# Kernel tuning notes

Hardware: AMD Instinct MI355X
Metric: run time of the kernel (lower is better)

Reference implementation:

```python
import jax, jax.numpy as jnp
import numpy as np

N = 50000        # num nodes
E = 1600000      # num edges (before self loops)
F_IN = 128
F_OUT = 64
SLOPE = 0.2      # PyG GATConv default negative_slope


def setup_inputs() -> dict:
    key = jax.random.key(0)
    k0, k1, k2, k3, k4, k5 = jax.random.split(key, 6)
    x = jax.random.normal(k0, (N, F_IN), dtype=jnp.float32)
    # GATConv params (heads=1): linear weight, attention vectors, bias
    W = jax.random.normal(k1, (F_IN, F_OUT), dtype=jnp.float32) * (1.0 / np.sqrt(F_IN))
    a_src = jax.random.normal(k2, (F_OUT,), dtype=jnp.float32) * (1.0 / np.sqrt(F_OUT))
    a_dst = jax.random.normal(k3, (F_OUT,), dtype=jnp.float32) * (1.0 / np.sqrt(F_OUT))
    bias = jax.random.normal(k4, (F_OUT,), dtype=jnp.float32) * 0.01
    edge_index = jax.random.randint(k5, (2, E), 0, N, dtype=jnp.int32)
    return {"x": x, "W": W, "a_src": a_src, "a_dst": a_dst, "bias": bias,
            "edge_index": edge_index}


def reference(x, W, a_src, a_dst, bias, edge_index):
    # Linear transform: [N, F_OUT]
    xp = x @ W
    # add self loops (PyG GATConv default add_self_loops=True)
    loop = jnp.arange(N, dtype=edge_index.dtype)
    src = jnp.concatenate([edge_index[0], loop])  # source j of edge j->i
    dst = jnp.concatenate([edge_index[1], loop])  # target i
    # per-node attention logits, gathered per edge
    alpha_s = xp @ a_src  # [N]
    alpha_d = xp @ a_dst  # [N]
    e = alpha_s[src] + alpha_d[dst]               # [E+N]
    e = jnp.where(e > 0, e, SLOPE * e)            # leaky_relu(0.2)
    # segment softmax over edges grouped by destination node
    emax = jax.ops.segment_max(e, dst, num_segments=N)  # every node has a self loop
    w = jnp.exp(e - emax[dst])
    denom = jax.ops.segment_sum(w, dst, num_segments=N)
    alpha = w / denom[dst]                        # [E+N]
    # scatter-aggregate weighted source features
    out = jax.ops.segment_sum(alpha[:, None] * xp[src], dst, num_segments=N)
    out = out + bias
    # F.relu then unsqueeze(dim=0) and cat with empty -> [1, N, F_OUT]
    return jax.nn.relu(out)[None, :, :]
```

## Files before the change

### kernel.cpp

```cpp
#include <hip/hip_runtime.h>
#include <hip/hip_fp16.h>
#include <math.h>

#define N_NODES 50000
#define N_EDGES 1600000
#define ET (N_EDGES + N_NODES)
#define F_OUT 64
#define F_IN 128
#define SLOPE 0.2f
#define BSHIFT 7
#define BNODES 128
#define NBUCK ((N_NODES + BNODES - 1) >> BSHIFT)
#define CAP 4736
#define EPB 4096
#define PBLOCKS ((ET + EPB - 1) / EPB)

typedef _Float16 half8 __attribute__((ext_vector_type(8)));
typedef _Float16 half4 __attribute__((ext_vector_type(4)));
typedef float f32x4 __attribute__((ext_vector_type(4)));

__global__ __launch_bounds__(256) void gemm_kernel(const float4* __restrict__ x4,
                                                   const float* __restrict__ W,
                                                   const float* __restrict__ a_src,
                                                   const float* __restrict__ a_dst,
                                                   _Float16* __restrict__ xph,
                                                   float* __restrict__ alpha_s,
                                                   float* __restrict__ alpha_d,
                                                   int* __restrict__ bcur) {
    __shared__ _Float16 xs[64][136];
    int t = threadIdx.x;
    if (blockIdx.x == 0)
        for (int i = t; i < NBUCK; i += 256) bcur[i] = 0;
    int wave = t >> 6, lane = t & 63;
    int g = lane >> 4, c16 = lane & 15;

    size_t rbase = (size_t)blockIdx.x * 64;
#pragma unroll
    for (int i = 0; i < 8; ++i) {
        int idx = t + i * 256;
        int row = idx >> 5, c4 = idx & 31;
        size_t gr = rbase + row;
        if (gr >= N_NODES) gr = N_NODES - 1;
        float4 v = x4[gr * (F_IN / 4) + c4];
        half4 hv = { (_Float16)v.x, (_Float16)v.y, (_Float16)v.z, (_Float16)v.w };
        *(half4*)&xs[row][c4 * 4] = hv;
    }

    half8 bw[4][4];
#pragma unroll
    for (int nt = 0; nt < 4; ++nt)
#pragma unroll
        for (int kt = 0; kt < 4; ++kt) {
            int col = nt * 16 + c16;
            int k0 = kt * 32 + g * 8;
#pragma unroll
            for (int e = 0; e < 8; ++e)
                bw[nt][kt][e] = (_Float16)W[(k0 + e) * F_OUT + col];
        }
    __syncthreads();

    int r0 = wave * 16;
    half8 af[4];
#pragma unroll
    for (int kt = 0; kt < 4; ++kt)
        af[kt] = *(const half8*)&xs[r0 + c16][kt * 32 + g * 8];

    f32x4 acc[4];
#pragma unroll
    for (int nt = 0; nt < 4; ++nt) {
        acc[nt] = (f32x4){0.f, 0.f, 0.f, 0.f};
#pragma unroll
        for (int kt = 0; kt < 4; ++kt)
            acc[nt] = __builtin_amdgcn_mfma_f32_16x16x32_f16(af[kt], bw[nt][kt], acc[nt], 0, 0, 0);
    }

    int growbase = (int)rbase + r0 + g * 4;
#pragma unroll
    for (int nt = 0; nt < 4; ++nt) {
#pragma unroll
        for (int r = 0; r < 4; ++r) {
            int row = growbase + r;
            if (row < N_NODES)
                xph[(size_t)row * F_OUT + nt * 16 + c16] = (_Float16)acc[nt][r];
        }
    }
    float asl[4], adl[4];
#pragma unroll
    for (int nt = 0; nt < 4; ++nt) {
        asl[nt] = a_src[nt * 16 + c16];
        adl[nt] = a_dst[nt * 16 + c16];
    }
#pragma unroll
    for (int r = 0; r < 4; ++r) {
        float ps = 0.f, pd = 0.f;
#pragma unroll
        for (int nt = 0; nt < 4; ++nt) {
            ps = fmaf(acc[nt][r], asl[nt], ps);
            pd = fmaf(acc[nt][r], adl[nt], pd);
        }
#pragma unroll
        for (int off = 1; off < 16; off <<= 1) {
            ps += __shfl_xor(ps, off);
            pd += __shfl_xor(pd, off);
        }
        int row = growbase + r;
        if (c16 == 0 && row < N_NODES) { alpha_s[row] = ps; alpha_d[row] = pd; }
    }
}

__global__ __launch_bounds__(256) void part_kernel(const int* __restrict__ ei,
                                                   int* __restrict__ bcur,
                                                   unsigned* __restrict__ rec) {
    __shared__ int lc[NBUCK];
    __shared__ int lbase[NBUCK];
    int t = threadIdx.x;
    for (int b = t; b < NBUCK; b += 256) lc[b] = 0;
    __syncthreads();
    int e0 = blockIdx.x * EPB;

    unsigned u[16]; short bk[16]; unsigned short rk[16];
#pragma unroll
    for (int k = 0; k < 4; ++k) {
        int e = e0 + k * 1024 + t * 4;
        int4 sv, dv;
        if (e + 3 < N_EDGES) {
            sv = *(const int4*)&ei[e];
            dv = *(const int4*)&ei[N_EDGES + e];
        } else {
            int* sp = (int*)&sv; int* dp = (int*)&dv;
#pragma unroll
            for (int j = 0; j < 4; ++j) {
                int ee = e + j;
                if (ee < N_EDGES)      { sp[j] = ei[ee]; dp[j] = ei[N_EDGES + ee]; }
                else if (ee < ET)      { sp[j] = dp[j] = ee - N_EDGES; }
                else                   { sp[j] = dp[j] = -1; }
            }
        }
        const int* sp = (const int*)&sv; const int* dp = (const int*)&dv;
#pragma unroll
        for (int j = 0; j < 4; ++j) {
            int i = k * 4 + j;
            int d = dp[j];
            if (d >= 0) {
                int b = d >> BSHIFT;
                bk[i] = (short)b;
                rk[i] = (unsigned short)atomicAdd(&lc[b], 1);
                u[i] = (unsigned)sp[j] | ((unsigned)d << 16);
            } else bk[i] = -1;
        }
    }
    __syncthreads();
    for (int b = t; b < NBUCK; b += 256)
        lbase[b] = lc[b] ? (b * CAP + atomicAdd(&bcur[b], lc[b])) : 0;
    __syncthreads();
#pragma unroll
    for (int i = 0; i < 16; ++i)
        if (bk[i] >= 0) rec[lbase[bk[i]] + rk[i]] = u[i];
}

__device__ __forceinline__ int block_incl_scan(int v, int t, int* wsum) {
    int lane = t & 63, wave = t >> 6;
#pragma unroll
    for (int off = 1; off < 64; off <<= 1) {
        int n = __shfl_up(v, off);
        if (lane >= off) v += n;
    }
    if (lane == 63) wsum[wave] = v;
    __syncthreads();
    int add = 0;
    for (int w = 0; w < wave; ++w) add += wsum[w];
    return v + add;
}

__global__ __launch_bounds__(512) void csrb_kernel(const unsigned* __restrict__ rec,
                                                   const int* __restrict__ bcur,
                                                   const float* __restrict__ as,
                                                   const float* __restrict__ ad,
                                                   int* __restrict__ offsets,
                                                   int* __restrict__ counts,
                                                   unsigned* __restrict__ wcsr) {
    __shared__ unsigned lrec[CAP];
    __shared__ int lcnt[BNODES], loff[BNODES], lcur[BNODES];
    __shared__ float adl[BNODES];
    __shared__ int wsum[8];
    int t = threadIdx.x;
    int b = blockIdx.x;
    int n0 = b << BSHIFT;
    int r0 = b * CAP;
    int cnt_b = bcur[b];
    if (t < BNODES) {
        lcnt[t] = 0; lcur[t] = 0;
        adl[t] = (n0 + t < N_NODES) ? ad[n0 + t] : 0.f;
    }
    for (int i = t; i < cnt_b; i += 512) lrec[i] = rec[r0 + i];
    __syncthreads();
    for (int i = t; i < cnt_b; i += 512)
        atomicAdd(&lcnt[(lrec[i] >> 16) & (BNODES - 1)], 1);
    __syncthreads();
    int v = (t < BNODES) ? lcnt[t] : 0;
    int incl = block_incl_scan(v, t, wsum);
    if (t < BNODES) {
        loff[t] = incl - v;
        if (n0 + t < N_NODES) { counts[n0 + t] = v; offsets[n0 + t] = r0 + incl - v; }
    }
    __syncthreads();
    for (int i = t; i < cnt_b; i += 512) {
        unsigned u = lrec[i];
        int dl = (u >> 16) & (BNODES - 1);
        int s = u & 0xFFFFu;
        float ev = as[s] + adl[dl];
        ev = ev > 0.f ? ev : SLOPE * ev;
        float w = __expf(ev);
        int pos = atomicAdd(&lcur[dl], 1);
        wcsr[r0 + loff[dl] + pos] =
            (unsigned)s | ((unsigned)__half_as_ushort(__float2half(w)) << 16);
    }
}

#define CONS(u_, h_)                                                           \
    {                                                                          \
        float w = __half2float(__ushort_as_half((unsigned short)((u_) >> 16)));\
        float2 p;                                                              \
        p = __half22float2(__builtin_bit_cast(__half2, (h_).x));               \
        a0 = fmaf(w, p.x, a0); a1 = fmaf(w, p.y, a1);                          \
        p = __half22float2(__builtin_bit_cast(__half2, (h_).y));               \
        a2 = fmaf(w, p.x, a2); a3 = fmaf(w, p.y, a3);                          \
        p = __half22float2(__builtin_bit_cast(__half2, (h_).z));               \
        a4 = fmaf(w, p.x, a4); a5 = fmaf(w, p.y, a5);                          \
        p = __half22float2(__builtin_bit_cast(__half2, (h_).w));               \
        a6 = fmaf(w, p.x, a6); a7 = fmaf(w, p.y, a7);                          \
        ws += w;                                                               \
    }

__global__ __launch_bounds__(256) void gather_kernel(const unsigned* __restrict__ wcsr,
                                                     const int* __restrict__ offsets,
                                                     const int* __restrict__ counts,
                                                     const __half* __restrict__ xp,
                                                     const float* __restrict__ bias,
                                                     float* __restrict__ out) {
    __shared__ unsigned stage[4][64];
    int wave = threadIdx.x >> 6, lane = threadIdx.x & 63;
    int d = blockIdx.x * 4 + wave;
    if (d >= N_NODES) return;
    int start = offsets[d], cnt = counts[d];
    int o = lane >> 3, f8 = lane & 7;
    const uint4* xp4 = (const uint4*)xp;
    float a0 = 0.f, a1 = 0.f, a2 = 0.f, a3 = 0.f;
    float a4 = 0.f, a5 = 0.f, a6 = 0.f, a7 = 0.f;
    float ws = 0.f;

    for (int jb = 0; jb < cnt; jb += 64) {
        int iters = min(cnt - jb, 64);
        stage[wave][lane] = (lane < iters) ? wcsr[start + jb + lane] : 0u;
        unsigned u0 = stage[wave][o];
        unsigned u1 = stage[wave][o + 8];
        unsigned u2 = stage[wave][o + 16];
        unsigned u3 = stage[wave][o + 24];
        unsigned u4 = stage[wave][o + 32];
        unsigned u5 = stage[wave][o + 40];
        unsigned u6 = stage[wave][o + 48];
        unsigned u7 = stage[wave][o + 56];
        uint4 h0 = xp4[(u0 & 0xFFFFu) * 8 + f8];
        uint4 h1 = xp4[(u1 & 0xFFFFu) * 8 + f8];
        uint4 h2 = xp4[(u2 & 0xFFFFu) * 8 + f8];
        uint4 h3 = xp4[(u3 & 0xFFFFu) * 8 + f8];
        uint4 h4 = xp4[(u4 & 0xFFFFu) * 8 + f8];
        uint4 h5 = xp4[(u5 & 0xFFFFu) * 8 + f8];
        uint4 h6 = xp4[(u6 & 0xFFFFu) * 8 + f8];
        uint4 h7 = xp4[(u7 & 0xFFFFu) * 8 + f8];
        CONS(u0, h0);
        CONS(u1, h1);
        CONS(u2, h2);
        CONS(u3, h3);
        CONS(u4, h4);
        CONS(u5, h5);
        CONS(u6, h6);
        CONS(u7, h7);
    }
#pragma unroll
    for (int off = 8; off < 64; off <<= 1) {
        a0 += __shfl_xor(a0, off);
        a1 += __shfl_xor(a1, off);
        a2 += __shfl_xor(a2, off);
        a3 += __shfl_xor(a3, off);
        a4 += __shfl_xor(a4, off);
        a5 += __shfl_xor(a5, off);
        a6 += __shfl_xor(a6, off);
        a7 += __shfl_xor(a7, off);
        ws += __shfl_xor(ws, off);
    }
    if (o == 0) {
        float inv = 1.f / ws;
        float4 b0 = ((const float4*)bias)[f8 * 2];
        float4 b1 = ((const float4*)bias)[f8 * 2 + 1];
        float4 o0, o1;
        o0.x = fmaf(a0, inv, b0.x); o0.y = fmaf(a1, inv, b0.y);
        o0.z = fmaf(a2, inv, b0.z); o0.w = fmaf(a3, inv, b0.w);
        o1.x = fmaf(a4, inv, b1.x); o1.y = fmaf(a5, inv, b1.y);
        o1.z = fmaf(a6, inv, b1.z); o1.w = fmaf(a7, inv, b1.w);
        o0.x = o0.x > 0.f ? o0.x : 0.f;
        o0.y = o0.y > 0.f ? o0.y : 0.f;
        o0.z = o0.z > 0.f ? o0.z : 0.f;
        o0.w = o0.w > 0.f ? o0.w : 0.f;
        o1.x = o1.x > 0.f ? o1.x : 0.f;
        o1.y = o1.y > 0.f ? o1.y : 0.f;
        o1.z = o1.z > 0.f ? o1.z : 0.f;
        o1.w = o1.w > 0.f ? o1.w : 0.f;
        ((float4*)out)[(size_t)d * 16 + f8 * 2]     = o0;
        ((float4*)out)[(size_t)d * 16 + f8 * 2 + 1] = o1;
    }
}

extern "C" void kernel_launch(void* const* d_in, const int* in_sizes, int n_in,
                              void* d_out, int out_size, void* d_ws, size_t ws_size,
                              hipStream_t stream) {
    const float* x     = (const float*)d_in[0];
    const float* W     = (const float*)d_in[1];
    const float* a_src = (const float*)d_in[2];
    const float* a_dst = (const float*)d_in[3];
    const float* bias  = (const float*)d_in[4];
    const int*   ei    = (const int*)d_in[5];
    float* out = (float*)d_out;

    _Float16* xph   = (_Float16*)d_ws;
    float*  as      = (float*)(xph + (size_t)N_NODES * F_OUT);
    float*  ad      = as + N_NODES;
    int*    counts  = (int*)(ad + N_NODES);
    int*    offsets = counts + N_NODES;
    int*    bcur    = offsets + N_NODES;
    unsigned* rec   = (unsigned*)(bcur + NBUCK + 64);
    unsigned* wcsr  = rec + (size_t)NBUCK * CAP;

    gemm_kernel<<<(N_NODES + 63) / 64, 256, 0, stream>>>(
        (const float4*)x, W, a_src, a_dst, xph, as, ad, bcur);
    part_kernel<<<PBLOCKS, 256, 0, stream>>>(ei, bcur, rec);
    csrb_kernel<<<NBUCK, 512, 0, stream>>>(rec, bcur, as, ad, offsets, counts, wcsr);
    gather_kernel<<<(N_NODES + 3) / 4, 256, 0, stream>>>(wcsr, offsets, counts,
                                                         (const __half*)xph, bias, out);
}
```

Baseline: 83.59 us.

## Shrink destination buckets to 32 nodes and simplify partition and CSR build

Destination buckets go from 128 to 32 nodes, and the per-bucket capacity and edges-per-block of the partition kernel shrink to match. The partition kernel now handles one int4 of edges per thread instead of four. The CSR-build kernel runs 256 threads per block, merges the record load with the histogram pass, and replaces the block scan with a single-wave shuffle scan. The intent is more, smaller CSR-build blocks for better occupancy and cheaper per-block work. The cost is that each partition block now touches far more buckets with few edges each, which raises global atomics and scatters record writes, and the smaller capacity leaves less slack for degree variance.

Measured after the change: 135.6 us. 1.62x slower.

```diff
diff --git a/kernel.cpp b/kernel.cpp
--- a/kernel.cpp
+++ b/kernel.cpp
@@ -8,11 +8,11 @@
 #define F_OUT 64
 #define F_IN 128
 #define SLOPE 0.2f
-#define BSHIFT 7
-#define BNODES 128
+#define BSHIFT 5
+#define BNODES 32
 #define NBUCK ((N_NODES + BNODES - 1) >> BSHIFT)
-#define CAP 4736
-#define EPB 4096
+#define CAP 1344
+#define EPB 1024
 #define PBLOCKS ((ET + EPB - 1) / EPB)
 
 typedef _Float16 half8 __attribute__((ext_vector_type(8)));
@@ -116,63 +116,44 @@
     int t = threadIdx.x;
     for (int b = t; b < NBUCK; b += 256) lc[b] = 0;
     __syncthreads();
-    int e0 = blockIdx.x * EPB;
-
-    unsigned u[16]; short bk[16]; unsigned short rk[16];
-#pragma unroll
-    for (int k = 0; k < 4; ++k) {
-        int e = e0 + k * 1024 + t * 4;
-        int4 sv, dv;
-        if (e + 3 < N_EDGES) {
-            sv = *(const int4*)&ei[e];
-            dv = *(const int4*)&ei[N_EDGES + e];
-        } else {
-            int* sp = (int*)&sv; int* dp = (int*)&dv;
-#pragma unroll
-            for (int j = 0; j < 4; ++j) {
-                int ee = e + j;
-                if (ee < N_EDGES)      { sp[j] = ei[ee]; dp[j] = ei[N_EDGES + ee]; }
-                else if (ee < ET)      { sp[j] = dp[j] = ee - N_EDGES; }
-                else                   { sp[j] = dp[j] = -1; }
-            }
-        }
-        const int* sp = (const int*)&sv; const int* dp = (const int*)&dv;
+
+    int e = blockIdx.x * EPB + t * 4;
+    int4 sv, dv;
+    if (e + 3 < N_EDGES) {
+        sv = *(const int4*)&ei[e];
+        dv = *(const int4*)&ei[N_EDGES + e];
+    } else {
+        int* sp = (int*)&sv; int* dp = (int*)&dv;
 #pragma unroll
         for (int j = 0; j < 4; ++j) {
-            int i = k * 4 + j;
-            int d = dp[j];
-            if (d >= 0) {
-                int b = d >> BSHIFT;
-                bk[i] = (short)b;
-                rk[i] = (unsigned short)atomicAdd(&lc[b], 1);
-                u[i] = (unsigned)sp[j] | ((unsigned)d << 16);
-            } else bk[i] = -1;
-        }
+            int ee = e + j;
+            if (ee < N_EDGES)      { sp[j] = ei[ee]; dp[j] = ei[N_EDGES + ee]; }
+            else if (ee < ET)      { sp[j] = dp[j] = ee - N_EDGES; }
+            else                   { sp[j] = dp[j] = -1; }
+        }
+    }
+    const int* sp = (const int*)&sv; const int* dp = (const int*)&dv;
+    unsigned u[4]; short bk[4]; unsigned short rk[4];
+#pragma unroll
+    for (int j = 0; j < 4; ++j) {
+        int d = dp[j];
+        if (d >= 0) {
+            int b = d >> BSHIFT;
+            bk[j] = (short)b;
+            rk[j] = (unsigned short)atomicAdd(&lc[b], 1);
+            u[j] = (unsigned)sp[j] | ((unsigned)d << 16);
+        } else bk[j] = -1;
     }
     __syncthreads();
     for (int b = t; b < NBUCK; b += 256)
-        lbase[b] = lc[b] ? (b * CAP + atomicAdd(&bcur[b], lc[b])) : 0;
-    __syncthreads();
-#pragma unroll
-    for (int i = 0; i < 16; ++i)
-        if (bk[i] >= 0) rec[lbase[bk[i]] + rk[i]] = u[i];
-}
-
-__device__ __forceinline__ int block_incl_scan(int v, int t, int* wsum) {
-    int lane = t & 63, wave = t >> 6;
-#pragma unroll
-    for (int off = 1; off < 64; off <<= 1) {
-        int n = __shfl_up(v, off);
-        if (lane >= off) v += n;
-    }
-    if (lane == 63) wsum[wave] = v;
-    __syncthreads();
-    int add = 0;
-    for (int w = 0; w < wave; ++w) add += wsum[w];
-    return v + add;
-}
-
-__global__ __launch_bounds__(512) void csrb_kernel(const unsigned* __restrict__ rec,
+        if (lc[b]) lbase[b] = b * CAP + atomicAdd(&bcur[b], lc[b]);
+    __syncthreads();
+#pragma unroll
+    for (int j = 0; j < 4; ++j)
+        if (bk[j] >= 0) rec[lbase[bk[j]] + rk[j]] = u[j];
+}
+
+__global__ __launch_bounds__(256) void csrb_kernel(const unsigned* __restrict__ rec,
                                                    const int* __restrict__ bcur,
                                                    const float* __restrict__ as,
                                                    const float* __restrict__ ad,
@@ -182,7 +163,6 @@
     __shared__ unsigned lrec[CAP];
     __shared__ int lcnt[BNODES], loff[BNODES], lcur[BNODES];
     __shared__ float adl[BNODES];
-    __shared__ int wsum[8];
     int t = threadIdx.x;
     int b = blockIdx.x;
     int n0 = b << BSHIFT;
@@ -192,19 +172,26 @@
         lcnt[t] = 0; lcur[t] = 0;
         adl[t] = (n0 + t < N_NODES) ? ad[n0 + t] : 0.f;
     }
-    for (int i = t; i < cnt_b; i += 512) lrec[i] = rec[r0 + i];
-    __syncthreads();
-    for (int i = t; i < cnt_b; i += 512)
-        atomicAdd(&lcnt[(lrec[i] >> 16) & (BNODES - 1)], 1);
-    __syncthreads();
-    int v = (t < BNODES) ? lcnt[t] : 0;
-    int incl = block_incl_scan(v, t, wsum);
+    __syncthreads();
+    for (int i = t; i < cnt_b; i += 256) {
+        unsigned u = rec[r0 + i];
+        lrec[i] = u;
+        atomicAdd(&lcnt[(u >> 16) & (BNODES - 1)], 1);
+    }
+    __syncthreads();
     if (t < BNODES) {
+        int v = lcnt[t];
+        int incl = v;
+#pragma unroll
+        for (int off = 1; off < BNODES; off <<= 1) {
+            int n = __shfl_up(incl, off);
+            if (t >= off) incl += n;
+        }
         loff[t] = incl - v;
         if (n0 + t < N_NODES) { counts[n0 + t] = v; offsets[n0 + t] = r0 + incl - v; }
     }
     __syncthreads();
-    for (int i = t; i < cnt_b; i += 512) {
+    for (int i = t; i < cnt_b; i += 256) {
         unsigned u = lrec[i];
         int dl = (u >> 16) & (BNODES - 1);
         int s = u & 0xFFFFu;
@@ -334,7 +321,7 @@
     gemm_kernel<<<(N_NODES + 63) / 64, 256, 0, stream>>>(
         (const float4*)x, W, a_src, a_dst, xph, as, ad, bcur);
     part_kernel<<<PBLOCKS, 256, 0, stream>>>(ei, bcur, rec);
-    csrb_kernel<<<NBUCK, 512, 0, stream>>>(rec, bcur, as, ad, offsets, counts, wcsr);
+    csrb_kernel<<<NBUCK, 256, 0, stream>>>(rec, bcur, as, ad, offsets, counts, wcsr);
     gather_kernel<<<(N_NODES + 3) / 4, 256, 0, stream>>>(wcsr, offsets, counts,
                                                          (const __half*)xph, bias, out);
 }
```
